# Optimization experiments

Hardware: AMD Instinct MI355X
Metric: run time of the kernel (lower is better)

The kernel has to match this reference:

```python
import jax, jax.numpy as jnp
import numpy as np

EPS = 1e-12  # matches torch F.normalize eps default scale behavior (1e-12)

def _l2_normalize(x):
    n = jnp.sqrt(jnp.sum(x * x, axis=-1, keepdims=True))
    return x / jnp.maximum(n, EPS)

def setup_inputs() -> dict:
    key = jax.random.key(0)
    k1, k2 = jax.random.split(key)
    B, K, D = 32768, 4096, 1024
    context_repr = jax.random.normal(k1, (B, D), dtype=jnp.float32)
    # matches nn.init.normal_(std=0.02)
    cluster_centers = 0.02 * jax.random.normal(k2, (K, D), dtype=jnp.float32)
    return {"context_repr": context_repr, "cluster_centers": cluster_centers}

def reference(context_repr, cluster_centers):
    # L2-normalize rows of both
    x = _l2_normalize(context_repr)        # [B, D]
    c = _l2_normalize(cluster_centers)     # [K, D]
    x2 = jnp.sum(x * x, axis=-1, keepdims=True)          # [B, 1]
    c2 = jnp.sum(c * c, axis=-1)[None, :]                # [1, K]
    d2 = x2 + c2 - 2.0 * jnp.einsum('bd,kd->bk', x, c)   # [B, K]
    hard = jnp.argmin(d2, axis=-1)                       # [B]
    # Gather the UN-normalized learnable centers (as in the torch code)
    cluster_embedding = cluster_centers[hard]            # [B, D]
    return cluster_embedding
```

## Files before the change

### kernel.cpp

```cpp
#include <hip/hip_runtime.h>
#include <stdint.h>

#define B_ROWS 32768
#define K_CENT 4096
#define D_DIM  1024
#define EPS_CAND 5e-4f

typedef unsigned short u16;
typedef __attribute__((ext_vector_type(8))) __bf16 bf16x8;
typedef __attribute__((ext_vector_type(4))) float f32x4;

__device__ inline u16 f32_to_bf16(float f) {
    unsigned u = __float_as_uint(f);
    u += 0x7FFFu + ((u >> 16) & 1u);
    return (u16)(u >> 16);
}
__device__ inline float bf16_to_f32(u16 h) {
    return __uint_as_float(((unsigned)h) << 16);
}
__device__ inline unsigned ord_of_f32(float f) {
    unsigned u = __float_as_uint(f);
    return (u & 0x80000000u) ? ~u : (u | 0x80000000u);
}
__device__ inline float f32_of_ord(unsigned o) {
    unsigned u = (o & 0x80000000u) ? (o & 0x7fffffffu) : ~o;
    return __uint_as_float(u);
}
__device__ inline void gload_lds16(const u16* g, u16* l) {
    __builtin_amdgcn_global_load_lds(
        (const __attribute__((address_space(1))) void*)g,
        (__attribute__((address_space(3))) void*)l, 16, 0, 0);
}

__global__ __launch_bounds__(256) void prep_rows(
    const float* __restrict__ src, u16* __restrict__ hi, u16* __restrict__ lo,
    float* __restrict__ sq, float* __restrict__ den)
{
    __shared__ double sm[4];
    const int row = blockIdx.x, tid = threadIdx.x;
    const float4 v = reinterpret_cast<const float4*>(src + (size_t)row * D_DIM)[tid];
    double ss = (double)v.x * v.x + (double)v.y * v.y
              + (double)v.z * v.z + (double)v.w * v.w;
#pragma unroll
    for (int m = 1; m < 64; m <<= 1) ss += __shfl_xor(ss, m, 64);
    if ((tid & 63) == 0) sm[tid >> 6] = ss;
    __syncthreads();
    const double tot = sm[0] + sm[1] + sm[2] + sm[3];
    const float d = fmaxf(sqrtf((float)tot), 1e-12f);
    const float n0 = v.x / d, n1 = v.y / d, n2 = v.z / d, n3 = v.w / d;

    ushort4 h, l;
    h.x = f32_to_bf16(n0); l.x = f32_to_bf16(n0 - bf16_to_f32(h.x));
    h.y = f32_to_bf16(n1); l.y = f32_to_bf16(n1 - bf16_to_f32(h.y));
    h.z = f32_to_bf16(n2); l.z = f32_to_bf16(n2 - bf16_to_f32(h.z));
    h.w = f32_to_bf16(n3); l.w = f32_to_bf16(n3 - bf16_to_f32(h.w));
    reinterpret_cast<ushort4*>(hi + (size_t)row * D_DIM)[tid] = h;
    reinterpret_cast<ushort4*>(lo + (size_t)row * D_DIM)[tid] = l;

    double s2 = (double)n0 * n0 + (double)n1 * n1
              + (double)n2 * n2 + (double)n3 * n3;
#pragma unroll
    for (int m = 1; m < 64; m <<= 1) s2 += __shfl_xor(s2, m, 64);
    __syncthreads();
    if ((tid & 63) == 0) sm[tid >> 6] = s2;
    __syncthreads();
    if (tid == 0) {
        sq[row] = (float)(sm[0] + sm[1] + sm[2] + sm[3]);
        den[row] = d;
    }
}

#define BM 256
#define BN 256
#define BK 64
#define NT 48
#define AREG 8192
#define BOFF_U16 16384
#define BUF_U16 32768

__global__ __launch_bounds__(512, 2) void gemm_cand(
    const u16* __restrict__ Ahi, const u16* __restrict__ Alo,
    const u16* __restrict__ Bhi, const u16* __restrict__ Blo,
    const float* __restrict__ c2, unsigned long long* __restrict__ cand)
{
    __shared__ u16 lds[2 * BUF_U16];

    const int tid = threadIdx.x, lane = tid & 63, w = tid >> 6;
    const int wm = w >> 2, wn = w & 3;
    const int fr = lane & 15, fc = lane >> 4;

    const int flat = blockIdx.x;
    const int swz = (flat & 7) * 256 + (flat >> 3);
    int bx = swz & 15;
    const int by = swz >> 4;
    if (by & 1) bx = 15 - bx;
    const size_t arow0 = (size_t)by * BM;
    const size_t brow0 = (size_t)bx * BN;

    const int prow = tid >> 2, pch = tid & 3;
    const int lc = pch ^ ((prow >> 1) & 3);
    const size_t lane0 = (size_t)prow * D_DIM + lc * 8;
    const size_t lane1 = (size_t)(prow + 128) * D_DIM + lc * 8;
    const int dst0 = tid * 8, dst1 = tid * 8 + 4096;
    const size_t abase = arow0 * D_DIM;
    const size_t bbase = brow0 * D_DIM;

#define STAGE_A(tn, jj) do {                                                  \
    const u16* s_ = ((((tn) >> 4) == 1) ? Alo : Ahi) + abase                  \
                    + ((size_t)((tn) & 15)) * BK + (jj) * 32;                 \
    u16* d_ = lds + ((tn) & 1) * BUF_U16 + (jj) * AREG;                       \
    gload_lds16(s_ + lane0, d_ + dst0);                                       \
    gload_lds16(s_ + lane1, d_ + dst1);                                       \
} while (0)
#define STAGE_B(tn, jj) do {                                                  \
    const u16* s_ = ((((tn) >> 4) == 2) ? Blo : Bhi) + bbase                  \
                    + ((size_t)((tn) & 15)) * BK + (jj) * 32;                 \
    u16* d_ = lds + ((tn) & 1) * BUF_U16 + BOFF_U16 + (jj) * AREG;            \
    gload_lds16(s_ + lane0, d_ + dst0);                                       \
    gload_lds16(s_ + lane1, d_ + dst1);                                       \
} while (0)

    int offA[8], offB[4];
#pragma unroll
    for (int i = 0; i < 8; ++i) {
        const int r = wm * 128 + i * 16 + fr;
        offA[i] = r * 32 + ((fc ^ ((r >> 1) & 3)) * 8);
    }
#pragma unroll
    for (int n = 0; n < 4; ++n) {
        const int r = wn * 64 + n * 16 + fr;
        offB[n] = r * 32 + ((fc ^ ((r >> 1) & 3)) * 8);
    }

    f32x4 acc[8][4] = {};

    STAGE_A(0, 0); STAGE_B(0, 0); STAGE_A(0, 1); STAGE_B(0, 1);
    asm volatile("s_waitcnt vmcnt(4)" ::: "memory");
    __builtin_amdgcn_s_barrier();
    __builtin_amdgcn_sched_barrier(0);

    for (int t = 0; t < NT; ++t) {
        const int cb = (t & 1) * BUF_U16;
        const u16* LA = lds + cb;
        const u16* LB = lds + cb + BOFF_U16;
        const int tn = t + 1;
        const bool st = tn < NT;

        bf16x8 af[4], bfr[4];

#pragma unroll
        for (int n = 0; n < 4; ++n)
            bfr[n] = *reinterpret_cast<const bf16x8*>(LB + offB[n]);
#pragma unroll
        for (int i = 0; i < 4; ++i)
            af[i] = *reinterpret_cast<const bf16x8*>(LA + offA[i]);
        if (st) STAGE_A(tn, 0);
        __builtin_amdgcn_sched_barrier(0);
        __builtin_amdgcn_s_barrier();
        __builtin_amdgcn_sched_barrier(0);
        __builtin_amdgcn_s_setprio(1);
#pragma unroll
        for (int i = 0; i < 4; ++i)
#pragma unroll
            for (int n = 0; n < 4; ++n)
                acc[i][n] = __builtin_amdgcn_mfma_f32_16x16x32_bf16(af[i], bfr[n], acc[i][n], 0, 0, 0);
        __builtin_amdgcn_s_setprio(0);
        __builtin_amdgcn_sched_barrier(0);
        __builtin_amdgcn_s_barrier();
        __builtin_amdgcn_sched_barrier(0);

#pragma unroll
        for (int i = 0; i < 4; ++i)
            af[i] = *reinterpret_cast<const bf16x8*>(LA + offA[4 + i]);
        if (st) STAGE_B(tn, 0);
        __builtin_amdgcn_sched_barrier(0);
        __builtin_amdgcn_s_barrier();
        __builtin_amdgcn_sched_barrier(0);
        __builtin_amdgcn_s_setprio(1);
#pragma unroll
        for (int i = 0; i < 4; ++i)
#pragma unroll
            for (int n = 0; n < 4; ++n)
                acc[4 + i][n] = __builtin_amdgcn_mfma_f32_16x16x32_bf16(af[i], bfr[n], acc[4 + i][n], 0, 0, 0);
        __builtin_amdgcn_s_setprio(0);
        if (t == NT - 1) asm volatile("s_waitcnt vmcnt(0)" ::: "memory");
        else             asm volatile("s_waitcnt vmcnt(4)" ::: "memory");
        __builtin_amdgcn_sched_barrier(0);
        __builtin_amdgcn_s_barrier();
        __builtin_amdgcn_sched_barrier(0);

#pragma unroll
        for (int n = 0; n < 4; ++n)
            bfr[n] = *reinterpret_cast<const bf16x8*>(LB + AREG + offB[n]);
#pragma unroll
        for (int i = 0; i < 4; ++i)
            af[i] = *reinterpret_cast<const bf16x8*>(LA + AREG + offA[i]);
        if (st) STAGE_A(tn, 1);
        __builtin_amdgcn_sched_barrier(0);
        __builtin_amdgcn_s_barrier();
        __builtin_amdgcn_sched_barrier(0);
        __builtin_amdgcn_s_setprio(1);
#pragma unroll
        for (int i = 0; i < 4; ++i)
#pragma unroll
            for (int n = 0; n < 4; ++n)
                acc[i][n] = __builtin_amdgcn_mfma_f32_16x16x32_bf16(af[i], bfr[n], acc[i][n], 0, 0, 0);
        __builtin_amdgcn_s_setprio(0);
        __builtin_amdgcn_sched_barrier(0);
        __builtin_amdgcn_s_barrier();
        __builtin_amdgcn_sched_barrier(0);

#pragma unroll
        for (int i = 0; i < 4; ++i)
            af[i] = *reinterpret_cast<const bf16x8*>(LA + AREG + offA[4 + i]);
        if (st) STAGE_B(tn, 1);
        __builtin_amdgcn_sched_barrier(0);
        __builtin_amdgcn_s_barrier();
        __builtin_amdgcn_sched_barrier(0);
        __builtin_amdgcn_s_setprio(1);
#pragma unroll
        for (int i = 0; i < 4; ++i)
#pragma unroll
            for (int n = 0; n < 4; ++n)
                acc[4 + i][n] = __builtin_amdgcn_mfma_f32_16x16x32_bf16(af[i], bfr[n], acc[4 + i][n], 0, 0, 0);
        __builtin_amdgcn_s_setprio(0);
        if (t < NT - 1) asm volatile("s_waitcnt vmcnt(4)" ::: "memory");
        __builtin_amdgcn_sched_barrier(0);
        __builtin_amdgcn_s_barrier();
        __builtin_amdgcn_sched_barrier(0);
    }
#undef STAGE_A
#undef STAGE_B

    const int group = bx * 4 + wn;
    float c2v[4];
#pragma unroll
    for (int n = 0; n < 4; ++n)
        c2v[n] = c2[brow0 + wn * 64 + n * 16 + fr];

#pragma unroll
    for (int mi = 0; mi < 8; ++mi) {
#pragma unroll
        for (int r = 0; r < 4; ++r) {
            unsigned long long bk = ~0ull;
#pragma unroll
            for (int ni = 0; ni < 4; ++ni) {
                const float d2a = c2v[ni] - 2.0f * acc[mi][ni][r];
                const unsigned col = (unsigned)(brow0 + wn * 64 + ni * 16 + fr);
                const unsigned long long key =
                    ((unsigned long long)ord_of_f32(d2a) << 32) | col;
                if (key < bk) bk = key;
            }
#pragma unroll
            for (int ms = 1; ms < 16; ms <<= 1) {
                const unsigned long long o = __shfl_xor(bk, ms, 64);
                if (o < bk) bk = o;
            }
            if (fr == 0) {
                const size_t grow = arow0 + wm * 128 + mi * 16 + fc * 4 + r;
                cand[grow * 64 + group] = bk;
            }
        }
    }
}

__global__ __launch_bounds__(256) void finalize(
    const unsigned long long* __restrict__ cand,
    const float* __restrict__ X, const float* __restrict__ C,
    const float* __restrict__ denx, const float* __restrict__ denc,
    const float* __restrict__ x2, const float* __restrict__ c2,
    float* __restrict__ out)
{
    const int w = threadIdx.x >> 6, lane = threadIdx.x & 63;
    const size_t row = (size_t)blockIdx.x * 4 + w;

    const unsigned long long v = cand[row * 64 + lane];
    unsigned long long m = v;
#pragma unroll
    for (int ms = 1; ms < 64; ms <<= 1) {
        const unsigned long long o = __shfl_xor(m, ms, 64);
        if (o < m) m = o;
    }
    const float fmin = f32_of_ord((unsigned)(m >> 32));
    const bool is_cand = f32_of_ord((unsigned)(v >> 32)) <= fmin + EPS_CAND;
    const unsigned long long ball = __ballot(is_cand);

    unsigned win;
    if (__popcll(ball) == 1) {
        win = (unsigned)(m & 0xffffffffu);
    } else {
        const float dxr = denx[row];
        const float x2r = x2[row];
        float xv[16];
#pragma unroll
        for (int j = 0; j < 16; ++j)
            xv[j] = X[row * D_DIM + j * 64 + lane] / dxr;

        float bestd2 = __uint_as_float(0x7f800000u);
        unsigned bwin = 0xffffffffu;
        unsigned long long bb = ball;
        while (bb) {
            const int l = __ffsll((unsigned long long)bb) - 1;
            bb &= bb - 1;
            const unsigned col = (unsigned)(__shfl(v, l, 64) & 0xffffffffu);
            const float dcr = denc[col];
            double s = 0.0;
#pragma unroll
            for (int j = 0; j < 16; ++j) {
                const float cv = C[(size_t)col * D_DIM + j * 64 + lane] / dcr;
                s = fma((double)xv[j], (double)cv, s);
            }
#pragma unroll
            for (int ms = 1; ms < 64; ms <<= 1) s += __shfl_xor(s, ms, 64);
            const float dotf = (float)s;
            const float d2 = (x2r + c2[col]) - 2.0f * dotf;
            if (d2 < bestd2 || (d2 == bestd2 && col < bwin)) {
                bestd2 = d2; bwin = col;
            }
        }
        win = bwin;
    }

    const float4* s4 = reinterpret_cast<const float4*>(C + (size_t)win * D_DIM);
    float4* d4 = reinterpret_cast<float4*>(out + row * D_DIM);
#pragma unroll
    for (int t = 0; t < 4; ++t) d4[t * 64 + lane] = s4[t * 64 + lane];
}

extern "C" void kernel_launch(void* const* d_in, const int* in_sizes, int n_in,
                              void* d_out, int out_size, void* d_ws, size_t ws_size,
                              hipStream_t stream)
{
    (void)in_sizes; (void)n_in; (void)out_size; (void)ws_size;
    const float* X = (const float*)d_in[0];
    const float* C = (const float*)d_in[1];
    float* out = (float*)d_out;

    char* ws = (char*)d_ws;
    u16* Ahi = (u16*)ws;
    u16* Alo = Ahi + (size_t)B_ROWS * D_DIM;
    u16* Bhi = Alo + (size_t)B_ROWS * D_DIM;
    u16* Blo = Bhi + (size_t)K_CENT * D_DIM;
    unsigned long long* cand =
        (unsigned long long*)(Blo + (size_t)K_CENT * D_DIM);
    float* c2   = (float*)(cand + (size_t)B_ROWS * 64);
    float* x2   = c2 + K_CENT;
    float* denx = x2 + B_ROWS;
    float* denc = denx + B_ROWS;

    prep_rows<<<B_ROWS, 256, 0, stream>>>(X, Ahi, Alo, x2, denx);
    prep_rows<<<K_CENT, 256, 0, stream>>>(C, Bhi, Blo, c2, denc);
    gemm_cand<<<(B_ROWS / BM) * (K_CENT / BN), 512, 0, stream>>>(
        Ahi, Alo, Bhi, Blo, c2, cand);
    finalize<<<B_ROWS / 4, 256, 0, stream>>>(
        cand, X, C, denx, denc, x2, c2, out);
}
```

Measured before the change: 990.8 us.

## Restructure GEMM main loop into 4-region ring with register double-buffered fragments

Replaces the two-buffer, four-barrier-per-tile loop with a four-slot LDS ring where each slot holds both A and B for a 32-wide K slice. Fragments for the next slice are loaded into alternate register sets while MFMAs consume the current set, leaving one barrier per phase. Loads are issued two slices ahead. Occupancy drops from 2 to 1 workgroup per CU because launch bounds change and register pressure rises with two fragment sets. The tight vmcnt/lgkmcnt accounting could race if the counts are wrong.

Result: slower. 1.040 ms (+5.0%).

```diff
diff --git a/kernel.cpp b/kernel.cpp
--- a/kernel.cpp
+++ b/kernel.cpp
@@ -72,18 +72,14 @@
 
 #define BM 256
 #define BN 256
-#define BK 64
-#define NT 48
-#define AREG 8192
-#define BOFF_U16 16384
-#define BUF_U16 32768
-
-__global__ __launch_bounds__(512, 2) void gemm_cand(
+#define REG_U16 16384
+
+__global__ __launch_bounds__(512, 1) void gemm_cand(
     const u16* __restrict__ Ahi, const u16* __restrict__ Alo,
     const u16* __restrict__ Bhi, const u16* __restrict__ Blo,
     const float* __restrict__ c2, unsigned long long* __restrict__ cand)
 {
-    __shared__ u16 lds[2 * BUF_U16];
+    __shared__ u16 lds[4 * REG_U16];
 
     const int tid = threadIdx.x, lane = tid & 63, w = tid >> 6;
     const int wm = w >> 2, wn = w & 3;
@@ -105,19 +101,15 @@
     const size_t abase = arow0 * D_DIM;
     const size_t bbase = brow0 * D_DIM;
 
-#define STAGE_A(tn, jj) do {                                                  \
-    const u16* s_ = ((((tn) >> 4) == 1) ? Alo : Ahi) + abase                  \
-                    + ((size_t)((tn) & 15)) * BK + (jj) * 32;                 \
-    u16* d_ = lds + ((tn) & 1) * BUF_U16 + (jj) * AREG;                       \
-    gload_lds16(s_ + lane0, d_ + dst0);                                       \
-    gload_lds16(s_ + lane1, d_ + dst1);                                       \
-} while (0)
-#define STAGE_B(tn, jj) do {                                                  \
-    const u16* s_ = ((((tn) >> 4) == 2) ? Blo : Bhi) + bbase                  \
-                    + ((size_t)((tn) & 15)) * BK + (jj) * 32;                 \
-    u16* d_ = lds + ((tn) & 1) * BUF_U16 + BOFF_U16 + (jj) * AREG;            \
-    gload_lds16(s_ + lane0, d_ + dst0);                                       \
-    gload_lds16(s_ + lane1, d_ + dst1);                                       \
+#define STAGE_R(tn, jj) do {                                                  \
+    u16* _d = lds + ((2 * (tn) + (jj)) & 3) * REG_U16;                        \
+    const size_t _k = (size_t)(((tn) & 15) * 64 + (jj) * 32);                 \
+    const u16* _sa = ((((tn) >> 4) == 1) ? Alo : Ahi) + abase + _k;           \
+    const u16* _sb = ((((tn) >> 4) == 2) ? Blo : Bhi) + bbase + _k;           \
+    gload_lds16(_sa + lane0, _d + dst0);                                      \
+    gload_lds16(_sa + lane1, _d + dst1);                                      \
+    gload_lds16(_sb + lane0, _d + 8192 + dst0);                               \
+    gload_lds16(_sb + lane1, _d + 8192 + dst1);                               \
 } while (0)
 
     int offA[8], offB[4];
@@ -133,104 +125,86 @@
     }
 
     f32x4 acc[8][4] = {};
-
-    STAGE_A(0, 0); STAGE_B(0, 0); STAGE_A(0, 1); STAGE_B(0, 1);
+    bf16x8 afE[8], bfE[4], afO[8], bfO[4];
+
+#define PHASE(RR, AFU, BFU, AFR, BFR, TST, JST, DOSTAGE, TRAILVM) do {        \
+    const u16* _r = lds + (RR) * REG_U16;                                     \
+    _Pragma("unroll")                                                         \
+    for (int _i = 0; _i < 8; ++_i)                                            \
+        AFR[_i] = *reinterpret_cast<const bf16x8*>(_r + offA[_i]);            \
+    _Pragma("unroll")                                                         \
+    for (int _n = 0; _n < 4; ++_n)                                            \
+        BFR[_n] = *reinterpret_cast<const bf16x8*>(_r + 8192 + offB[_n]);     \
+    __builtin_amdgcn_sched_barrier(0);                                        \
+    if (DOSTAGE) STAGE_R(TST, JST);                                           \
+    __builtin_amdgcn_sched_barrier(0);                                        \
+    __builtin_amdgcn_s_setprio(1);                                            \
+    _Pragma("unroll")                                                         \
+    for (int _i = 0; _i < 8; ++_i)                                            \
+        _Pragma("unroll")                                                     \
+        for (int _n = 0; _n < 4; ++_n)                                        \
+            acc[_i][_n] = __builtin_amdgcn_mfma_f32_16x16x32_bf16(            \
+                AFU[_i], BFU[_n], acc[_i][_n], 0, 0, 0);                      \
+    __builtin_amdgcn_s_setprio(0);                                            \
+    __builtin_amdgcn_sched_barrier(0);                                        \
+    asm volatile("s_waitcnt vmcnt(" TRAILVM ") lgkmcnt(12)" ::: "memory");    \
+    __builtin_amdgcn_sched_barrier(0);                                        \
+    __builtin_amdgcn_s_barrier();                                             \
+} while (0)
+
+    STAGE_R(0, 0); STAGE_R(0, 1); STAGE_R(1, 0);
     asm volatile("s_waitcnt vmcnt(4)" ::: "memory");
+    __builtin_amdgcn_sched_barrier(0);
     __builtin_amdgcn_s_barrier();
+    {
+        const u16* _r = lds;
+#pragma unroll
+        for (int i = 0; i < 8; ++i)
+            afE[i] = *reinterpret_cast<const bf16x8*>(_r + offA[i]);
+#pragma unroll
+        for (int n = 0; n < 4; ++n)
+            bfE[n] = *reinterpret_cast<const bf16x8*>(_r + 8192 + offB[n]);
+    }
     __builtin_amdgcn_sched_barrier(0);
 
-    for (int t = 0; t < NT; ++t) {
-        const int cb = (t & 1) * BUF_U16;
-        const u16* LA = lds + cb;
-        const u16* LB = lds + cb + BOFF_U16;
-        const int tn = t + 1;
-        const bool st = tn < NT;
-
-        bf16x8 af[4], bfr[4];
-
+    for (int s = 0; s < 23; ++s) {
+        const int t2 = 2 * s;
+        PHASE(1, afE, bfE, afO, bfO, t2 + 1, 1, true, "4");
+        PHASE(2, afO, bfO, afE, bfE, t2 + 2, 0, true, "4");
+        PHASE(3, afE, bfE, afO, bfO, t2 + 2, 1, true, "4");
+        PHASE(0, afO, bfO, afE, bfE, t2 + 3, 0, true, "4");
+    }
+    PHASE(1, afE, bfE, afO, bfO, 47, 1, true,  "4");
+    PHASE(2, afO, bfO, afE, bfE, 0,  0, false, "0");
+    {
+        const u16* _r = lds + 3 * REG_U16;
+#pragma unroll
+        for (int i = 0; i < 8; ++i)
+            afO[i] = *reinterpret_cast<const bf16x8*>(_r + offA[i]);
 #pragma unroll
         for (int n = 0; n < 4; ++n)
-            bfr[n] = *reinterpret_cast<const bf16x8*>(LB + offB[n]);
-#pragma unroll
-        for (int i = 0; i < 4; ++i)
-            af[i] = *reinterpret_cast<const bf16x8*>(LA + offA[i]);
-        if (st) STAGE_A(tn, 0);
-        __builtin_amdgcn_sched_barrier(0);
-        __builtin_amdgcn_s_barrier();
-        __builtin_amdgcn_sched_barrier(0);
+            bfO[n] = *reinterpret_cast<const bf16x8*>(_r + 8192 + offB[n]);
         __builtin_amdgcn_s_setprio(1);
 #pragma unroll
-        for (int i = 0; i < 4; ++i)
+        for (int i = 0; i < 8; ++i)
 #pragma unroll
             for (int n = 0; n < 4; ++n)
-                acc[i][n] = __builtin_amdgcn_mfma_f32_16x16x32_bf16(af[i], bfr[n], acc[i][n], 0, 0, 0);
+                acc[i][n] = __builtin_amdgcn_mfma_f32_16x16x32_bf16(
+                    afE[i], bfE[n], acc[i][n], 0, 0, 0);
         __builtin_amdgcn_s_setprio(0);
-        __builtin_amdgcn_sched_barrier(0);
-        __builtin_amdgcn_s_barrier();
-        __builtin_amdgcn_sched_barrier(0);
-
-#pragma unroll
-        for (int i = 0; i < 4; ++i)
-            af[i] = *reinterpret_cast<const bf16x8*>(LA + offA[4 + i]);
-        if (st) STAGE_B(tn, 0);
-        __builtin_amdgcn_sched_barrier(0);
-        __builtin_amdgcn_s_barrier();
-        __builtin_amdgcn_sched_barrier(0);
+    }
+    {
         __builtin_amdgcn_s_setprio(1);
 #pragma unroll
-        for (int i = 0; i < 4; ++i)
+        for (int i = 0; i < 8; ++i)
 #pragma unroll
             for (int n = 0; n < 4; ++n)
-                acc[4 + i][n] = __builtin_amdgcn_mfma_f32_16x16x32_bf16(af[i], bfr[n], acc[4 + i][n], 0, 0, 0);
+                acc[i][n] = __builtin_amdgcn_mfma_f32_16x16x32_bf16(
+                    afO[i], bfO[n], acc[i][n], 0, 0, 0);
         __builtin_amdgcn_s_setprio(0);
-        if (t == NT - 1) asm volatile("s_waitcnt vmcnt(0)" ::: "memory");
-        else             asm volatile("s_waitcnt vmcnt(4)" ::: "memory");
-        __builtin_amdgcn_sched_barrier(0);
-        __builtin_amdgcn_s_barrier();
-        __builtin_amdgcn_sched_barrier(0);
-
-#pragma unroll
-        for (int n = 0; n < 4; ++n)
-            bfr[n] = *reinterpret_cast<const bf16x8*>(LB + AREG + offB[n]);
-#pragma unroll
-        for (int i = 0; i < 4; ++i)
-            af[i] = *reinterpret_cast<const bf16x8*>(LA + AREG + offA[i]);
-        if (st) STAGE_A(tn, 1);
-        __builtin_amdgcn_sched_barrier(0);
-        __builtin_amdgcn_s_barrier();
-        __builtin_amdgcn_sched_barrier(0);
-        __builtin_amdgcn_s_setprio(1);
-#pragma unroll
-        for (int i = 0; i < 4; ++i)
-#pragma unroll
-            for (int n = 0; n < 4; ++n)
-                acc[i][n] = __builtin_amdgcn_mfma_f32_16x16x32_bf16(af[i], bfr[n], acc[i][n], 0, 0, 0);
-        __builtin_amdgcn_s_setprio(0);
-        __builtin_amdgcn_sched_barrier(0);
-        __builtin_amdgcn_s_barrier();
-        __builtin_amdgcn_sched_barrier(0);
-
-#pragma unroll
-        for (int i = 0; i < 4; ++i)
-            af[i] = *reinterpret_cast<const bf16x8*>(LA + AREG + offA[4 + i]);
-        if (st) STAGE_B(tn, 1);
-        __builtin_amdgcn_sched_barrier(0);
-        __builtin_amdgcn_s_barrier();
-        __builtin_amdgcn_sched_barrier(0);
-        __builtin_amdgcn_s_setprio(1);
-#pragma unroll
-        for (int i = 0; i < 4; ++i)
-#pragma unroll
-            for (int n = 0; n < 4; ++n)
-                acc[4 + i][n] = __builtin_amdgcn_mfma_f32_16x16x32_bf16(af[i], bfr[n], acc[4 + i][n], 0, 0, 0);
-        __builtin_amdgcn_s_setprio(0);
-        if (t < NT - 1) asm volatile("s_waitcnt vmcnt(4)" ::: "memory");
-        __builtin_amdgcn_sched_barrier(0);
-        __builtin_amdgcn_s_barrier();
-        __builtin_amdgcn_sched_barrier(0);
-    }
-#undef STAGE_A
-#undef STAGE_B
+    }
+#undef PHASE
+#undef STAGE_R
 
     const int group = bx * 4 + wn;
     float c2v[4];
```
